# Performance work log

Hardware: AMD Instinct MI355X
Metric: run time of the kernel (lower is better)

The kernel has to match this reference:

```python
import jax, jax.numpy as jnp
import numpy as np

N = 20000
E = 640000
D = 128


def setup_inputs() -> dict:
    key = jax.random.key(0)
    ks = jax.random.split(key, 8)
    x = jax.random.normal(ks[0], (N, D), dtype=jnp.float32)
    edge_index = jax.random.randint(ks[1], (2, E), 0, N, dtype=jnp.int64)
    s = 1.0 / np.sqrt(D)
    inp = {"x": x, "edge_index": edge_index}
    for i, layer in enumerate([2, 4, 6]):
        inp[f"W{i+1}"] = jax.random.uniform(ks[layer], (D, D), jnp.float32, -s, s)
        inp[f"b{i+1}"] = jax.random.uniform(ks[layer + 1], (D,), jnp.float32, -s, s)
    return inp


def _gcn_layer(x, src, dst, deg_inv, W, b):
    # linear (torch convention: y = x @ W.T + b), W: [out, in]
    xt = x @ W.T + b
    # gather source-node features, scatter-mean onto targets
    msg = xt[src]                                   # [E, D]
    agg = jax.ops.segment_sum(msg, dst, num_segments=N)  # [N, D]
    agg = agg * deg_inv[:, None]                    # mean over incoming edges
    return jax.nn.relu(agg) + xt


def reference(x, edge_index, W1, b1, W2, b2, W3, b3):
    src, dst = edge_index[0], edge_index[1]
    deg = jax.ops.segment_sum(jnp.ones((E,), jnp.float32), dst, num_segments=N)
    deg_inv = jnp.where(deg > 0, 1.0 / jnp.maximum(deg, 1.0), 0.0)
    for W, b in ((W1, b1), (W2, b2), (W3, b3)):
        x = _gcn_layer(x, src, dst, deg_inv, W, b)
    return x
```

## Files before the change

### kernel.cpp

```cpp
#include <hip/hip_runtime.h>

#define DD 128
#define KC 32
#define MT 64
#define ELLC 128
#define NBMAX 320
#define ACAP 2304
#define AEPW 4096

__device__ __forceinline__ unsigned f2bf_rne(float f) {
    unsigned u = __float_as_uint(f);
    u += 0x7fffu + ((u >> 16) & 1u);
    return u >> 16;
}

__device__ __forceinline__ void gemm_body(float (*Xs)[MT + 4], float (*Ws)[DD + 4],
                                          const float* x,
                                          const float* __restrict__ W,
                                          const float* __restrict__ b,
                                          float* xt,
                                          unsigned* __restrict__ xtb, int M, int PS, int blk) {
    const int tid  = threadIdx.x;
    const int cg_  = tid & 15;
    const int rg   = tid >> 4;
    const int row0 = blk * MT;

    float acc[4][8];
#pragma unroll
    for (int i = 0; i < 4; ++i)
#pragma unroll
        for (int j = 0; j < 8; ++j) acc[i][j] = 0.0f;

    for (int kc = 0; kc < DD; kc += KC) {
#pragma unroll
        for (int it = 0; it < 2; ++it) {
            int idx = tid + it * 256;
            int r = idx >> 3, kq = idx & 7;
            int gr = row0 + r;
            float4 v = make_float4(0.f, 0.f, 0.f, 0.f);
            if (gr < M) v = *(const float4*)&x[gr * DD + kc + kq * 4];
            Xs[kq * 4 + 0][r] = v.x; Xs[kq * 4 + 1][r] = v.y;
            Xs[kq * 4 + 2][r] = v.z; Xs[kq * 4 + 3][r] = v.w;
        }
#pragma unroll
        for (int it = 0; it < 4; ++it) {
            int idx = tid + it * 256;
            int o = idx >> 3, kq = idx & 7;
            float4 v = *(const float4*)&W[o * DD + kc + kq * 4];
            Ws[kq * 4 + 0][o] = v.x; Ws[kq * 4 + 1][o] = v.y;
            Ws[kq * 4 + 2][o] = v.z; Ws[kq * 4 + 3][o] = v.w;
        }
        __syncthreads();

#pragma unroll 8
        for (int k = 0; k < KC; ++k) {
            float4 xv = *(const float4*)&Xs[k][rg * 4];
            float4 w0 = *(const float4*)&Ws[k][cg_ * 8];
            float4 w1 = *(const float4*)&Ws[k][cg_ * 8 + 4];
            float xr[4] = {xv.x, xv.y, xv.z, xv.w};
            float wc[8] = {w0.x, w0.y, w0.z, w0.w, w1.x, w1.y, w1.z, w1.w};
#pragma unroll
            for (int i = 0; i < 4; ++i)
#pragma unroll
                for (int j = 0; j < 8; ++j) acc[i][j] += xr[i] * wc[j];
        }
        __syncthreads();
    }

    float4 b0 = *(const float4*)&b[cg_ * 8];
    float4 b1 = *(const float4*)&b[cg_ * 8 + 4];
    float bb[8] = {b0.x, b0.y, b0.z, b0.w, b1.x, b1.y, b1.z, b1.w};
#pragma unroll
    for (int i = 0; i < 4; ++i) {
        int gr = row0 + rg * 4 + i;
        if (gr < M) {
            float v[8];
#pragma unroll
            for (int j = 0; j < 8; ++j) v[j] = acc[i][j] + bb[j];
            *(float4*)&xt[gr * DD + cg_ * 8]     = make_float4(v[0], v[1], v[2], v[3]);
            *(float4*)&xt[gr * DD + cg_ * 8 + 4] = make_float4(v[4], v[5], v[6], v[7]);
            uint4 p;
            p.x = f2bf_rne(v[0]) | (f2bf_rne(v[1]) << 16);
            p.y = f2bf_rne(v[2]) | (f2bf_rne(v[3]) << 16);
            p.z = f2bf_rne(v[4]) | (f2bf_rne(v[5]) << 16);
            p.w = f2bf_rne(v[6]) | (f2bf_rne(v[7]) << 16);
            unsigned* xp = xtb + (size_t)(cg_ >> 3) * ((size_t)PS * 32)
                               + (size_t)gr * 32 + ((cg_ & 7) << 2);
            *(uint4*)xp = p;
        }
    }
}

__global__ __launch_bounds__(256) void gemm_xwT(const float* x,
                                                const float* __restrict__ W,
                                                const float* __restrict__ b,
                                                float* xt,
                                                unsigned* __restrict__ xtb, int M, int PS) {
    __shared__ float Xs[KC][MT + 4];
    __shared__ float Ws[KC][DD + 4];
    gemm_body(Xs, Ws, x, W, b, xt, xtb, M, PS, blockIdx.x);
}

__global__ __launch_bounds__(256) void gemm1_plus_binA(const float* x,
                                                       const float* __restrict__ W,
                                                       const float* __restrict__ b,
                                                       float* xt,
                                                       unsigned* __restrict__ xtb, int M, int PS,
                                                       const int* __restrict__ src,
                                                       const int* __restrict__ dst,
                                                       int* __restrict__ bucket_count,
                                                       unsigned* __restrict__ bstore,
                                                       int E, int NB, int PA) {
    __shared__ float Xs[KC][MT + 4];
    __shared__ float Ws[KC][DD + 4];
    __shared__ int hist[NBMAX];
    __shared__ int basec[NBMAX];
    __shared__ int cur[NBMAX];

    if ((int)blockIdx.x >= PA) {
        gemm_body(Xs, Ws, x, W, b, xt, xtb, M, PS, blockIdx.x - PA);
        return;
    }

    const int tid = threadIdx.x;
    for (int i = tid; i < NB; i += 256) hist[i] = 0;
    __syncthreads();

    int dv[16], sv[16];
    const int ebase = blockIdx.x * AEPW;
#pragma unroll
    for (int r = 0; r < 4; ++r) {
        int e = ebase + r * 1024 + tid * 4;
        if (e + 4 <= E) {
            int4 d4 = *(const int4*)&dst[e];
            int4 s4 = *(const int4*)&src[e];
            dv[r*4+0] = d4.x; dv[r*4+1] = d4.y; dv[r*4+2] = d4.z; dv[r*4+3] = d4.w;
            sv[r*4+0] = s4.x; sv[r*4+1] = s4.y; sv[r*4+2] = s4.z; sv[r*4+3] = s4.w;
        } else {
#pragma unroll
            for (int q = 0; q < 4; ++q) {
                int ee = e + q;
                if (ee < E) { dv[r*4+q] = dst[ee]; sv[r*4+q] = src[ee]; }
                else        { dv[r*4+q] = -1;      sv[r*4+q] = 0; }
            }
        }
    }
#pragma unroll
    for (int i = 0; i < 16; ++i)
        if (dv[i] >= 0) atomicAdd(&hist[dv[i] >> 6], 1);
    __syncthreads();

    for (int bk = tid; bk < NB; bk += 256) {
        int h = hist[bk];
        basec[bk] = h ? atomicAdd(&bucket_count[bk], h) : 0;
        cur[bk] = 0;
    }
    __syncthreads();

#pragma unroll
    for (int i = 0; i < 16; ++i) {
        if (dv[i] >= 0) {
            int bk = dv[i] >> 6;
            int pos = basec[bk] + atomicAdd(&cur[bk], 1);
            if (pos < ACAP)
                bstore[bk * ACAP + pos] = ((unsigned)(dv[i] & 63) << 16) | (unsigned)sv[i];
        }
    }
}

__global__ __launch_bounds__(256) void ell_build(const unsigned* __restrict__ bstore,
                                                 const int* __restrict__ bucket_count,
                                                 unsigned short* __restrict__ colell,
                                                 int* __restrict__ deg,
                                                 unsigned* __restrict__ xtb,
                                                 int PS, int N) {
    __shared__ int c64[64];
    const int bk = blockIdx.x;
    for (int i = threadIdx.x; i < 64; i += 256) c64[i] = 0;
    __syncthreads();
    int cnt = bucket_count[bk];
    if (cnt > ACAP) cnt = ACAP;
    for (int i = threadIdx.x; i < cnt; i += 256) {
        unsigned code = bstore[bk * ACAP + i];
        int local = (int)(code >> 16);
        int s     = (int)(code & 0xffffu);
        int p = atomicAdd(&c64[local], 1);
        if (p < ELLC)
            colell[((((bk << 6) + local)) << 7) + p] = (unsigned short)s;
    }
    __syncthreads();
    if (threadIdx.x < 64) {
        int node = (bk << 6) + threadIdx.x;
        if (node < N) {
            int d = c64[threadIdx.x];
            deg[node] = d;
            int stored = d < ELLC ? d : ELLC;
            int padded = (stored + 3) & ~3;
            if (padded > ELLC) padded = ELLC;
            unsigned short* row = colell + ((size_t)node << 7);
            for (int p2 = stored; p2 < padded; ++p2) row[p2] = (unsigned short)N;
        }
    }
    if (bk == 0 && threadIdx.x >= 64 && threadIdx.x < 80) {
        int i  = threadIdx.x - 64;
        int pl = i >> 3;
        int j  = i & 7;
        *(uint4*)&xtb[((size_t)pl * PS + (size_t)N) * 32 + (size_t)j * 4] =
            make_uint4(0u, 0u, 0u, 0u);
    }
}

__global__ __launch_bounds__(256) void gcn_aggregate(const uint2* __restrict__ xtb2,
                                                     const float* xt,
                                                     const unsigned short* __restrict__ colell,
                                                     const int* __restrict__ deg,
                                                     float* out, int PS, int N) {
    const int wave = threadIdx.x >> 6;
    const int lane = threadIdx.x & 63;
    const int node = (int)blockIdx.x * 4 + wave;
    if (node >= N) return;
    const int h = lane & 15;
    const int q = lane >> 4;

    const uint2* __restrict__ xl0 = xtb2 + h;
    const uint2* __restrict__ xl1 = xtb2 + ((size_t)PS << 4) + h;
    const unsigned short* __restrict__ crow = colell + ((size_t)node << 7);
    const int cnt = deg[node];
    const int cl  = cnt < ELLC ? cnt : ELLC;

    float a0 = 0.f, a1 = 0.f, a2 = 0.f, a3 = 0.f;
    float a4 = 0.f, a5 = 0.f, a6 = 0.f, a7 = 0.f;

#define GATH2(j_) { int s_ = __shfl(myidx, ((t + (j_)) << 2) | q, 64); \
                    u0[j_] = xl0[(size_t)s_ << 4]; \
                    u1[j_] = xl1[(size_t)s_ << 4]; }
#define UNPK2(j_) { a0 += __uint_as_float(u0[j_].x << 16); \
                    a1 += __uint_as_float(u0[j_].x & 0xffff0000u); \
                    a2 += __uint_as_float(u0[j_].y << 16); \
                    a3 += __uint_as_float(u0[j_].y & 0xffff0000u); \
                    a4 += __uint_as_float(u1[j_].x << 16); \
                    a5 += __uint_as_float(u1[j_].x & 0xffff0000u); \
                    a6 += __uint_as_float(u1[j_].y << 16); \
                    a7 += __uint_as_float(u1[j_].y & 0xffff0000u); }

    for (int base = 0; base < cl; base += 64) {
        const int rem = cl - base;
        const int c = rem < 64 ? rem : 64;
        const int myidx = (int)crow[base + lane];
        const int cq = (c + 3) >> 2;
        int t = 0;
        for (; t + 8 <= cq; t += 8) {
            uint2 u0[8], u1[8];
            GATH2(0) GATH2(1) GATH2(2) GATH2(3)
            GATH2(4) GATH2(5) GATH2(6) GATH2(7)
            UNPK2(0) UNPK2(1) UNPK2(2) UNPK2(3)
            UNPK2(4) UNPK2(5) UNPK2(6) UNPK2(7)
        }
        for (; t < cq; ++t) {
            uint2 u0[1], u1[1];
            GATH2(0)
            UNPK2(0)
        }
    }
#undef GATH2
#undef UNPK2

    a0 += __shfl_down(a0, 32, 64); a1 += __shfl_down(a1, 32, 64);
    a2 += __shfl_down(a2, 32, 64); a3 += __shfl_down(a3, 32, 64);
    a4 += __shfl_down(a4, 32, 64); a5 += __shfl_down(a5, 32, 64);
    a6 += __shfl_down(a6, 32, 64); a7 += __shfl_down(a7, 32, 64);
    a0 += __shfl_down(a0, 16, 64); a1 += __shfl_down(a1, 16, 64);
    a2 += __shfl_down(a2, 16, 64); a3 += __shfl_down(a3, 16, 64);
    a4 += __shfl_down(a4, 16, 64); a5 += __shfl_down(a5, 16, 64);
    a6 += __shfl_down(a6, 16, 64); a7 += __shfl_down(a7, 16, 64);

    if (q == 0) {
        const float di = (cnt > 0) ? (1.0f / (float)cnt) : 0.0f;
        float4 tA = ((const float4*)xt)[(size_t)node * 32 + h];
        float4 tB = ((const float4*)xt)[(size_t)node * 32 + 16 + h];
        float4 oA, oB;
        oA.x = fmaxf(a0 * di, 0.f) + tA.x;
        oA.y = fmaxf(a1 * di, 0.f) + tA.y;
        oA.z = fmaxf(a2 * di, 0.f) + tA.z;
        oA.w = fmaxf(a3 * di, 0.f) + tA.w;
        oB.x = fmaxf(a4 * di, 0.f) + tB.x;
        oB.y = fmaxf(a5 * di, 0.f) + tB.y;
        oB.z = fmaxf(a6 * di, 0.f) + tB.z;
        oB.w = fmaxf(a7 * di, 0.f) + tB.w;
        ((float4*)out)[(size_t)node * 32 + h]      = oA;
        ((float4*)out)[(size_t)node * 32 + 16 + h] = oB;
    }
}

extern "C" void kernel_launch(void* const* d_in, const int* in_sizes, int n_in,
                              void* d_out, int out_size, void* d_ws, size_t ws_size,
                              hipStream_t stream) {
    const float* x  = (const float*)d_in[0];
    const int*   ei = (const int*)d_in[1];
    const float* W1 = (const float*)d_in[2];
    const float* b1 = (const float*)d_in[3];
    const float* W2 = (const float*)d_in[4];
    const float* b2 = (const float*)d_in[5];
    const float* W3 = (const float*)d_in[6];
    const float* b3 = (const float*)d_in[7];

    const int N  = in_sizes[0] / DD;
    const int E  = in_sizes[1] / 2;
    const int PS = N + 1;

    const int* src = ei;
    const int* dst = ei + E;

    const int NB = (N + 63) >> 6;
    const int PA = (E + AEPW - 1) / AEPW;
    const int GB = (N + MT - 1) / MT;
    const int AB = (N + 3) / 4;

    char* ws = (char*)d_ws;
    size_t off = 0;
    auto alloc = [&](size_t bytes) {
        void* p = ws + off;
        off += (bytes + 255) & ~(size_t)255;
        return p;
    };
    int*            bucket_count = (int*)alloc((size_t)NB * sizeof(int));
    unsigned*       bstore       = (unsigned*)alloc((size_t)NB * ACAP * sizeof(unsigned));
    unsigned short* colell       = (unsigned short*)alloc((size_t)NB * 64 * ELLC * sizeof(unsigned short));
    int*            deg          = (int*)alloc((size_t)N * sizeof(int));
    unsigned*       xtb          = (unsigned*)alloc((size_t)PS * 256);

    float* xbuf = (float*)d_out;

    hipMemsetAsync(bucket_count, 0, (size_t)NB * sizeof(int), stream);
    gemm1_plus_binA<<<PA + GB, 256, 0, stream>>>(x, W1, b1, xbuf, xtb, N, PS,
                                                 src, dst, bucket_count, bstore, E, NB, PA);
    ell_build<<<NB, 256, 0, stream>>>(bstore, bucket_count, colell, deg, xtb, PS, N);

    gcn_aggregate<<<AB, 256, 0, stream>>>((const uint2*)xtb, xbuf, colell, deg, xbuf, PS, N);

    gemm_xwT<<<GB, 256, 0, stream>>>(xbuf, W2, b2, xbuf, xtb, N, PS);
    gcn_aggregate<<<AB, 256, 0, stream>>>((const uint2*)xtb, xbuf, colell, deg, xbuf, PS, N);

    gemm_xwT<<<GB, 256, 0, stream>>>(xbuf, W3, b3, xbuf, xtb, N, PS);
    gcn_aggregate<<<AB, 256, 0, stream>>>((const uint2*)xtb, xbuf, colell, deg, xbuf, PS, N);
}
```

Baseline: 226.8 us.

## Split aggregation per feature half with persistent waves and prefetched ELL rows

The aggregate kernel now gives each wave one half of a node's features (one bf16 plane) instead of the whole node. Waves loop persistently over 2N tasks in a fixed grid. Each wave prefetches the next task's ELL row while the current gathers are in flight. The in-degree is packed into the last slot of each ELL row, which removes the separate deg array and its load, and rows are now capped at 124 neighbours. Per-wave work drops to 4 accumulators, which raises occupancy, but each neighbour index is now read and shuffled twice.

```diff
diff --git a/kernel.cpp b/kernel.cpp
--- a/kernel.cpp
+++ b/kernel.cpp
@@ -4,9 +4,11 @@
 #define KC 32
 #define MT 64
 #define ELLC 128
+#define ELLI 124
 #define NBMAX 320
 #define ACAP 2304
 #define AEPW 4096
+#define AGGB 2048
 
 __device__ __forceinline__ unsigned f2bf_rne(float f) {
     unsigned u = __float_as_uint(f);
@@ -171,7 +173,6 @@
 __global__ __launch_bounds__(256) void ell_build(const unsigned* __restrict__ bstore,
                                                  const int* __restrict__ bucket_count,
                                                  unsigned short* __restrict__ colell,
-                                                 int* __restrict__ deg,
                                                  unsigned* __restrict__ xtb,
                                                  int PS, int N) {
     __shared__ int c64[64];
@@ -185,7 +186,7 @@
         int local = (int)(code >> 16);
         int s     = (int)(code & 0xffffu);
         int p = atomicAdd(&c64[local], 1);
-        if (p < ELLC)
+        if (p < ELLI)
             colell[((((bk << 6) + local)) << 7) + p] = (unsigned short)s;
     }
     __syncthreads();
@@ -193,12 +194,11 @@
         int node = (bk << 6) + threadIdx.x;
         if (node < N) {
             int d = c64[threadIdx.x];
-            deg[node] = d;
-            int stored = d < ELLC ? d : ELLC;
+            int stored = d < ELLI ? d : ELLI;
             int padded = (stored + 3) & ~3;
-            if (padded > ELLC) padded = ELLC;
             unsigned short* row = colell + ((size_t)node << 7);
             for (int p2 = stored; p2 < padded; ++p2) row[p2] = (unsigned short)N;
+            row[127] = (unsigned short)(d < 65535 ? d : 65535);
         }
     }
     if (bk == 0 && threadIdx.x >= 64 && threadIdx.x < 80) {
@@ -210,85 +210,90 @@
     }
 }
 
-__global__ __launch_bounds__(256) void gcn_aggregate(const uint2* __restrict__ xtb2,
-                                                     const float* xt,
-                                                     const unsigned short* __restrict__ colell,
-                                                     const int* __restrict__ deg,
-                                                     float* out, int PS, int N) {
-    const int wave = threadIdx.x >> 6;
+__global__ __launch_bounds__(256, 8) void gcn_aggregate(const uint2* __restrict__ xtb2,
+                                                        const float* xt,
+                                                        const unsigned* __restrict__ colell32,
+                                                        float* out, int PS, int N) {
     const int lane = threadIdx.x & 63;
-    const int node = (int)blockIdx.x * 4 + wave;
-    if (node >= N) return;
+    const int wid  = (int)blockIdx.x * 4 + (threadIdx.x >> 6);
+    const int NW   = (int)gridDim.x * 4;
+    const int T    = 2 * N;
+    if (wid >= T) return;
     const int h = lane & 15;
     const int q = lane >> 4;
 
-    const uint2* __restrict__ xl0 = xtb2 + h;
-    const uint2* __restrict__ xl1 = xtb2 + ((size_t)PS << 4) + h;
-    const unsigned short* __restrict__ crow = colell + ((size_t)node << 7);
-    const int cnt = deg[node];
-    const int cl  = cnt < ELLC ? cnt : ELLC;
-
-    float a0 = 0.f, a1 = 0.f, a2 = 0.f, a3 = 0.f;
-    float a4 = 0.f, a5 = 0.f, a6 = 0.f, a7 = 0.f;
-
-#define GATH2(j_) { int s_ = __shfl(myidx, ((t + (j_)) << 2) | q, 64); \
-                    u0[j_] = xl0[(size_t)s_ << 4]; \
-                    u1[j_] = xl1[(size_t)s_ << 4]; }
-#define UNPK2(j_) { a0 += __uint_as_float(u0[j_].x << 16); \
-                    a1 += __uint_as_float(u0[j_].x & 0xffff0000u); \
-                    a2 += __uint_as_float(u0[j_].y << 16); \
-                    a3 += __uint_as_float(u0[j_].y & 0xffff0000u); \
-                    a4 += __uint_as_float(u1[j_].x << 16); \
-                    a5 += __uint_as_float(u1[j_].x & 0xffff0000u); \
-                    a6 += __uint_as_float(u1[j_].y << 16); \
-                    a7 += __uint_as_float(u1[j_].y & 0xffff0000u); }
-
-    for (int base = 0; base < cl; base += 64) {
-        const int rem = cl - base;
-        const int c = rem < 64 ? rem : 64;
-        const int myidx = (int)crow[base + lane];
-        const int cq = (c + 3) >> 2;
-        int t = 0;
-        for (; t + 8 <= cq; t += 8) {
-            uint2 u0[8], u1[8];
-            GATH2(0) GATH2(1) GATH2(2) GATH2(3)
-            GATH2(4) GATH2(5) GATH2(6) GATH2(7)
-            UNPK2(0) UNPK2(1) UNPK2(2) UNPK2(3)
-            UNPK2(4) UNPK2(5) UNPK2(6) UNPK2(7)
-        }
-        for (; t < cq; ++t) {
-            uint2 u0[1], u1[1];
-            GATH2(0)
-            UNPK2(0)
-        }
-    }
-#undef GATH2
-#undef UNPK2
-
-    a0 += __shfl_down(a0, 32, 64); a1 += __shfl_down(a1, 32, 64);
-    a2 += __shfl_down(a2, 32, 64); a3 += __shfl_down(a3, 32, 64);
-    a4 += __shfl_down(a4, 32, 64); a5 += __shfl_down(a5, 32, 64);
-    a6 += __shfl_down(a6, 32, 64); a7 += __shfl_down(a7, 32, 64);
-    a0 += __shfl_down(a0, 16, 64); a1 += __shfl_down(a1, 16, 64);
-    a2 += __shfl_down(a2, 16, 64); a3 += __shfl_down(a3, 16, 64);
-    a4 += __shfl_down(a4, 16, 64); a5 += __shfl_down(a5, 16, 64);
-    a6 += __shfl_down(a6, 16, 64); a7 += __shfl_down(a7, 16, 64);
-
-    if (q == 0) {
-        const float di = (cnt > 0) ? (1.0f / (float)cnt) : 0.0f;
-        float4 tA = ((const float4*)xt)[(size_t)node * 32 + h];
-        float4 tB = ((const float4*)xt)[(size_t)node * 32 + 16 + h];
-        float4 oA, oB;
-        oA.x = fmaxf(a0 * di, 0.f) + tA.x;
-        oA.y = fmaxf(a1 * di, 0.f) + tA.y;
-        oA.z = fmaxf(a2 * di, 0.f) + tA.z;
-        oA.w = fmaxf(a3 * di, 0.f) + tA.w;
-        oB.x = fmaxf(a4 * di, 0.f) + tB.x;
-        oB.y = fmaxf(a5 * di, 0.f) + tB.y;
-        oB.z = fmaxf(a6 * di, 0.f) + tB.z;
-        oB.w = fmaxf(a7 * di, 0.f) + tB.w;
-        ((float4*)out)[(size_t)node * 32 + h]      = oA;
-        ((float4*)out)[(size_t)node * 32 + 16 + h] = oB;
+    int t = wid;
+    int node0 = (t >= N) ? t - N : t;
+    unsigned pk = colell32[((size_t)node0 << 6) + lane];
+
+    while (t < T) {
+        const int tn    = t + NW;
+        const int node  = (t >= N) ? t - N : t;
+        const int plane = (t >= N) ? 1 : 0;
+        const uint2* __restrict__ xl = xtb2 + (size_t)plane * ((size_t)PS << 4) + h;
+
+        const unsigned w63 = __shfl(pk, 63, 64);
+        const int cnt = (int)(w63 >> 16);
+        const int cl  = cnt < ELLI ? cnt : ELLI;
+        const int cq  = (cl + 3) >> 2;
+
+        float4 t4 = make_float4(0.f, 0.f, 0.f, 0.f);
+        if (q == 0)
+            t4 = ((const float4*)xt)[(size_t)node * 32 + plane * 16 + h];
+
+        float a0 = 0.f, a1 = 0.f, a2 = 0.f, a3 = 0.f;
+        unsigned pkn = 0;
+        bool first = true;
+
+        int tq = 0;
+        while (tq < cq) {
+            int f = cq - tq; if (f > 8) f = 8;
+            uint2 u[8];
+#pragma unroll
+            for (int j = 0; j < 8; ++j) if (j < f) {
+                int e = ((tq + j) << 2) | q;
+                unsigned w = __shfl(pk, e >> 1, 64);
+                int s = (e & 1) ? (int)(w >> 16) : (int)(w & 0xffffu);
+                u[j] = xl[(size_t)s << 4];
+            }
+            if (first) {
+                if (tn < T) {
+                    int nnode = (tn >= N) ? tn - N : tn;
+                    pkn = colell32[((size_t)nnode << 6) + lane];
+                }
+                first = false;
+            }
+#pragma unroll
+            for (int j = 0; j < 8; ++j) if (j < f) {
+                a0 += __uint_as_float(u[j].x << 16);
+                a1 += __uint_as_float(u[j].x & 0xffff0000u);
+                a2 += __uint_as_float(u[j].y << 16);
+                a3 += __uint_as_float(u[j].y & 0xffff0000u);
+            }
+            tq += f;
+        }
+        if (first && tn < T) {
+            int nnode = (tn >= N) ? tn - N : tn;
+            pkn = colell32[((size_t)nnode << 6) + lane];
+        }
+
+        a0 += __shfl_down(a0, 32, 64); a1 += __shfl_down(a1, 32, 64);
+        a2 += __shfl_down(a2, 32, 64); a3 += __shfl_down(a3, 32, 64);
+        a0 += __shfl_down(a0, 16, 64); a1 += __shfl_down(a1, 16, 64);
+        a2 += __shfl_down(a2, 16, 64); a3 += __shfl_down(a3, 16, 64);
+
+        if (q == 0) {
+            const float di = (cnt > 0) ? (1.0f / (float)cnt) : 0.0f;
+            float4 o;
+            o.x = fmaxf(a0 * di, 0.f) + t4.x;
+            o.y = fmaxf(a1 * di, 0.f) + t4.y;
+            o.z = fmaxf(a2 * di, 0.f) + t4.z;
+            o.w = fmaxf(a3 * di, 0.f) + t4.w;
+            ((float4*)out)[(size_t)node * 32 + plane * 16 + h] = o;
+        }
+
+        t = tn;
+        pk = pkn;
     }
 }
 
@@ -314,7 +319,6 @@
     const int NB = (N + 63) >> 6;
     const int PA = (E + AEPW - 1) / AEPW;
     const int GB = (N + MT - 1) / MT;
-    const int AB = (N + 3) / 4;
 
     char* ws = (char*)d_ws;
     size_t off = 0;
@@ -326,7 +330,6 @@
     int*            bucket_count = (int*)alloc((size_t)NB * sizeof(int));
     unsigned*       bstore       = (unsigned*)alloc((size_t)NB * ACAP * sizeof(unsigned));
     unsigned short* colell       = (unsigned short*)alloc((size_t)NB * 64 * ELLC * sizeof(unsigned short));
-    int*            deg          = (int*)alloc((size_t)N * sizeof(int));
     unsigned*       xtb          = (unsigned*)alloc((size_t)PS * 256);
 
     float* xbuf = (float*)d_out;
@@ -334,13 +337,16 @@
     hipMemsetAsync(bucket_count, 0, (size_t)NB * sizeof(int), stream);
     gemm1_plus_binA<<<PA + GB, 256, 0, stream>>>(x, W1, b1, xbuf, xtb, N, PS,
                                                  src, dst, bucket_count, bstore, E, NB, PA);
-    ell_build<<<NB, 256, 0, stream>>>(bstore, bucket_count, colell, deg, xtb, PS, N);
-
-    gcn_aggregate<<<AB, 256, 0, stream>>>((const uint2*)xtb, xbuf, colell, deg, xbuf, PS, N);
+    ell_build<<<NB, 256, 0, stream>>>(bstore, bucket_count, colell, xtb, PS, N);
+
+    gcn_aggregate<<<AGGB, 256, 0, stream>>>((const uint2*)xtb, xbuf,
+                                            (const unsigned*)colell, xbuf, PS, N);
 
     gemm_xwT<<<GB, 256, 0, stream>>>(xbuf, W2, b2, xbuf, xtb, N, PS);
-    gcn_aggregate<<<AB, 256, 0, stream>>>((const uint2*)xtb, xbuf, colell, deg, xbuf, PS, N);
+    gcn_aggregate<<<AGGB, 256, 0, stream>>>((const uint2*)xtb, xbuf,
+                                            (const unsigned*)colell, xbuf, PS, N);
 
     gemm_xwT<<<GB, 256, 0, stream>>>(xbuf, W3, b3, xbuf, xtb, N, PS);
-    gcn_aggregate<<<AB, 256, 0, stream>>>((const uint2*)xtb, xbuf, colell, deg, xbuf, PS, N);
-}
+    gcn_aggregate<<<AGGB, 256, 0, stream>>>((const uint2*)xtb, xbuf,
+                                            (const unsigned*)colell, xbuf, PS, N);
+}
```

New measurement: 208.8 us, median of 2. 7.9% less time.
